# Kernel tuning notes

Measured on AMD Instinct MI355X. Metric: run time of the kernel, lower is better.

The kernel has to match this reference:

```python
import jax, jax.numpy as jnp
import numpy as np

B, L, LQ = 64, 4096, 128
D = 32        # input_dim (value channels)
ET = 128      # embed_time
NH = 1        # num_heads
H = 128       # nhidden
NC = 6        # n_classes


def _time_emb(tt, lin_w, lin_b, per_w, per_b):
    # tt [..., T] -> [..., T, ET]; cat(Linear(1,1)(t), sin(Linear(1,ET-1)(t)))
    tt = tt[..., None]
    out1 = tt * lin_w[0, 0] + lin_b
    out2 = jnp.sin(tt @ per_w + per_b)
    return jnp.concatenate([out1, out2], axis=-1)


def _gru_dir(xs, wih, whh, bih, bhh, reverse):
    # xs [B, T, I] -> [B, T, H]; torch GRU gate math
    xs_t = jnp.swapaxes(xs, 0, 1)              # [T, B, I]
    if reverse:
        xs_t = xs_t[::-1]
    gi_all = xs_t @ wih.T + bih                # [T, B, 3H] precomputed input gates
    h0 = jnp.zeros((xs.shape[0], H), xs.dtype)

    def step(h, gi):
        gh = h @ whh.T + bhh
        ir, iz, inn = jnp.split(gi, 3, axis=-1)
        hr, hz, hn = jnp.split(gh, 3, axis=-1)
        r = jax.nn.sigmoid(ir + hr)
        z = jax.nn.sigmoid(iz + hz)
        n = jnp.tanh(inn + r * hn)
        h_new = (1.0 - z) * n + z * h
        return h_new, h_new

    _, ys = jax.lax.scan(step, h0, gi_all)     # [T, B, H]
    if reverse:
        ys = ys[::-1]
    return jnp.swapaxes(ys, 0, 1)


def _bigru(xs, wih, whh, bih, bhh):
    fwd = _gru_dir(xs, wih[0], whh[0], bih[0], bhh[0], False)
    bwd = _gru_dir(xs, wih[1], whh[1], bih[1], bhh[1], True)
    return jnp.concatenate([fwd, bwd], axis=-1)


def setup_inputs() -> dict:
    ks = jax.random.split(jax.random.key(0), 32)
    w = lambda i, s: jax.random.normal(ks[i], s, jnp.float32) * 0.05
    G3 = 3 * H
    return {
        "x": jax.random.normal(ks[0], (B, L, D), jnp.float32),
        "time_steps": jax.random.uniform(ks[1], (B, L), dtype=jnp.float32),
        "query_times": jnp.linspace(0.0, 1.0, LQ, dtype=jnp.float32),
        "lin_w": w(2, (1, 1)), "lin_b": w(3, (1,)),
        "per_w": w(4, (1, ET - 1)), "per_b": w(5, (ET - 1,)),
        "wq": w(6, (ET, ET)), "bq": w(7, (ET,)),
        "wk": w(8, (ET, ET)), "bk": w(9, (ET,)),
        "wo": w(10, (NH * D, H)), "bo": w(11, (H,)),
        "gru0_wih": w(12, (2, G3, H)), "gru0_whh": w(13, (2, G3, H)),
        "gru0_bih": w(14, (2, G3)), "gru0_bhh": w(15, (2, G3)),
        "gru1_wih": w(16, (2, G3, 2 * H)), "gru1_whh": w(17, (2, G3, H)),
        "gru1_bih": w(18, (2, G3)), "gru1_bhh": w(19, (2, G3)),
        "c1_w": w(20, (2 * H, 128)), "c1_b": w(21, (128,)),
        "c2_w": w(22, (128, 64)), "c2_b": w(23, (64,)),
        "c3_w": w(24, (64, NC)), "c3_b": w(25, (NC,)),
    }


def reference(x, time_steps, query_times, lin_w, lin_b, per_w, per_b,
              wq, bq, wk, bk, wo, bo,
              gru0_wih, gru0_whh, gru0_bih, gru0_bhh,
              gru1_wih, gru1_whh, gru1_bih, gru1_bhh,
              c1_w, c1_b, c2_w, c2_b, c3_w, c3_b):
    ek = ET // NH
    # learned time embeddings
    q = _time_emb(query_times[None, :], lin_w, lin_b, per_w, per_b)  # [1, LQ, ET]
    k = _time_emb(time_steps, lin_w, lin_b, per_w, per_b)            # [B, L, ET]
    # per-head projections
    qp = (q @ wq + bq).reshape(1, LQ, NH, ek).transpose(0, 2, 1, 3)[0]  # [NH, LQ, ek]
    kp = (k @ wk + bk).reshape(B, L, NH, ek).transpose(0, 2, 1, 3)      # [B, NH, L, ek]
    # mTAN attention: scores are channel-independent (mask=None), so the
    # per-channel repeat+softmax reduces to a single softmax over keys.
    scores = jnp.einsum('hqe,bhke->bhqk', qp, kp) / jnp.sqrt(jnp.float32(ek))
    p = jax.nn.softmax(scores, axis=-1)                                 # [B, NH, LQ, L]
    att = jnp.einsum('bhqk,bkd->bqhd', p, x).reshape(B, LQ, NH * D)
    att_out = att @ wo + bo                                             # [B, LQ, H]
    # 2-layer bidirectional GRU
    g0 = _bigru(att_out, gru0_wih, gru0_whh, gru0_bih, gru0_bhh)        # [B, LQ, 2H]
    g1 = _bigru(g0, gru1_wih, gru1_whh, gru1_bih, gru1_bhh)             # [B, LQ, 2H]
    class_in = jnp.concatenate([g1[:, -1, :H], g1[:, 0, H:]], axis=1)   # [B, 2H]
    out = ((class_in @ c1_w + c1_b) @ c2_w + c2_b) @ c3_w + c3_b        # [B, NC]
    return out
```

## Files before the change

kernel.cpp:

```cpp
#include <hip/hip_runtime.h>
#include <math.h>

#define Bn   64
#define Ln   4096
#define LQn  128
#define Dn   32
#define ETn  128
#define Hn   128
#define G3n  384
#define NDEG 12

typedef __attribute__((ext_vector_type(2))) float f32x2;
typedef __attribute__((ext_vector_type(2))) _Float16 f16x2;

#define DPPF(x, ctrl) __int_as_float(__builtin_amdgcn_update_dpp(0, __float_as_int(x), (ctrl), 0xF, 0xF, true))
#define QP_XOR1 0xB1
#define QP_XOR2 0x4E
#define QP_B0   0x00
#define QP_B1   0x55
#define QP_B2   0xAA
#define QP_B3   0xFF

__device__ __forceinline__ float sin_poly(float x) {
    const float x2 = x * x;
    float r = -1.9841270114e-04f;
    r = fmaf(r, x2,  8.3333337680e-03f);
    r = fmaf(r, x2, -1.6666667163e-01f);
    return fmaf(r * x2, x, x);
}
__device__ __forceinline__ float cos_poly(float x) {
    const float x2 = x * x;
    float r =  2.4801587642e-05f;
    r = fmaf(r, x2, -1.3888888899e-03f);
    r = fmaf(r, x2,  4.1666667908e-02f);
    r = fmaf(r, x2, -5.0000000000e-01f);
    return fmaf(r, x2, 1.0f);
}

#define WS_C    0
#define WS_WT   4096
#define WS_B2   (WS_WT + 768*32)
#define WS_CLS  (WS_B2 + 1024)
#define WS_G0   (WS_CLS + Bn*2*Hn)
#define WS_GI   (WS_G0 + Bn*LQn*2*Hn)
#define WS_ACCP WS_G0
#define WS_SP   (WS_G0 + 1048576)

__global__ __launch_bounds__(128) void k_coef(
    const float* __restrict__ qtimes, const float* __restrict__ lin_w,
    const float* __restrict__ lin_b, const float* __restrict__ per_w,
    const float* __restrict__ per_b, const float* __restrict__ wq,
    const float* __restrict__ bq, const float* __restrict__ wk,
    const float* __restrict__ bk, float* __restrict__ C)
{
    __shared__ float qe[ETn], qp_l[ETn], qt_l[ETn], bas[NDEG * 128], red[96], qbk_red[32];
    const int q = blockIdx.x, tid = threadIdx.x;
    if (tid < ETn - 1) {
        const float w = per_w[tid], bb = per_b[tid];
        const float sb = sin_poly(bb), cb = cos_poly(bb);
        float wp = 1.f;
#pragma unroll
        for (int d = 0; d < NDEG; ++d) {
            const float sd = ((d & 3) == 0) ? sb : ((d & 3) == 1) ? cb : ((d & 3) == 2) ? -sb : -cb;
            bas[d * 128 + tid] = wp * sd;
            wp *= w / (float)(d + 1);
        }
    }
    const float t = qtimes[q];
    qe[tid] = (tid == 0) ? fmaf(t, lin_w[0], lin_b[0])
                         : sin_poly(fmaf(t, per_w[tid - 1], per_b[tid - 1]));
    __syncthreads();
    {
        float a = bq[tid];
#pragma unroll 16
        for (int i = 0; i < ETn; ++i) a = fmaf(qe[i], wq[i * ETn + tid], a);
        qp_l[tid] = a;
    }
    __syncthreads();
    {
        const float4* wk4 = (const float4*)(wk + (size_t)tid * ETn);
        const float4* qp4 = (const float4*)qp_l;
        float a = 0.f;
#pragma unroll
        for (int k = 0; k < 32; ++k) {
            const float4 w4 = wk4[k], p4 = qp4[k];
            a += w4.x * p4.x + w4.y * p4.y + w4.z * p4.z + w4.w * p4.w;
        }
        qt_l[tid] = a;
    }
    __syncthreads();
    if (tid < 96) {
        const int d = tid >> 3, g = tid & 7;
        float p = 0.f;
        for (int j = g; j < ETn - 1; j += 8) p = fmaf(qt_l[j + 1], bas[d * 128 + j], p);
        red[tid] = p;
    } else {
        const int g2 = tid - 96;
        float p = 0.f;
#pragma unroll
        for (int k = 0; k < 4; ++k) p = fmaf(qp_l[g2 + 32 * k], bk[g2 + 32 * k], p);
        qbk_red[g2] = p;
    }
    __syncthreads();
    if (tid < NDEG) {
        const int d = tid;
        float s = red[d * 8 + 0] + red[d * 8 + 1] + red[d * 8 + 2] + red[d * 8 + 3]
                + red[d * 8 + 4] + red[d * 8 + 5] + red[d * 8 + 6] + red[d * 8 + 7];
        if (d == 0) {
            float qbk = 0.f;
#pragma unroll
            for (int k = 0; k < 32; ++k) qbk += qbk_red[k];
            s += qt_l[0] * lin_b[0] + qbk;
        }
        if (d == 1) s += qt_l[0] * lin_w[0];
        C[q * NDEG + d] = s * 0.08838834764831845f;
    }
}

__global__ __launch_bounds__(256) void k_fuse(
    const float* __restrict__ wih, const float* __restrict__ wo,
    const float* __restrict__ bo, const float* __restrict__ bih,
    float* __restrict__ Wt, float* __restrict__ bias2)
{
    const int t = blockIdx.x * 256 + threadIdx.x;
    if (t < 768 * 32) {
        const int o = t >> 5, d = t & 31;
        const float4* wr4 = (const float4*)(wih + (size_t)o * 128);
        const float4* wc4 = (const float4*)(wo + (size_t)d * 128);
        float a = 0.f;
#pragma unroll
        for (int k = 0; k < 32; ++k) {
            const float4 r4 = wr4[k], c4 = wc4[k];
            a += r4.x * c4.x + r4.y * c4.y + r4.z * c4.z + r4.w * c4.w;
        }
        Wt[t] = a;
    } else if (t < 768 * 33) {
        const int o = t - 768 * 32;
        const float4* wr4 = (const float4*)(wih + (size_t)o * 128);
        const float4* bo4 = (const float4*)bo;
        float a = bih[o];
#pragma unroll
        for (int k = 0; k < 32; ++k) {
            const float4 r4 = wr4[k], b4 = bo4[k];
            a += r4.x * b4.x + r4.y * b4.y + r4.z * b4.z + r4.w * b4.w;
        }
        bias2[o] = a;
    }
}

__global__ __launch_bounds__(512, 1) void k_attn(
    const float* __restrict__ x, const float* __restrict__ tsteps,
    const float* __restrict__ Cc, float* __restrict__ accP, float* __restrict__ sP)
{
    __shared__ float4 xls[4 * 64 * 8];
    __shared__ float  slab[4][128][36];
    const int tid = threadIdx.x;
    const int b = blockIdx.x >> 2, lsplit = blockIdx.x & 3;
    const int i = tid & 3, qt = (tid >> 2) & 31, ls2 = tid >> 7;
    const int qown = 4 * qt + i;
    const int u = tid & 127;

    float c[NDEG];
#pragma unroll
    for (int d = 0; d < NDEG; ++d) c[d] = Cc[qown * NDEG + d];

    const int l0 = lsplit * 1024 + ls2 * 256;
    const float4* tg4 = (const float4*)(tsteps + (size_t)b * Ln + l0);
    const float4* xg  = (const float4*)(x + ((size_t)b * Ln + l0) * Dn);

    f32x2 acc2[4][4];
#pragma unroll
    for (int m = 0; m < 4; ++m)
#pragma unroll
        for (int e = 0; e < 4; ++e) { acc2[m][e].x = 0.f; acc2[m][e].y = 0.f; }
    float s_own = 0.f;

    float4 xr[4];
#pragma unroll
    for (int w = 0; w < 4; ++w) xr[w] = xg[u + 128 * w];

    for (int ch = 0; ch < 4; ++ch) {
        __syncthreads();
#pragma unroll
        for (int w = 0; w < 4; ++w) xls[ls2 * 512 + u + 128 * w] = xr[w];
        __syncthreads();
        if (ch < 3) {
            const int off = (ch + 1) * 512;
#pragma unroll
            for (int w = 0; w < 4; ++w) xr[w] = xg[off + u + 128 * w];
        }
        const float4* xrow = &xls[ls2 * 512];
        for (int k = 0; k < 16; ++k) {
            const float4 t4 = tg4[ch * 16 + k];
#pragma unroll
            for (int jj = 0; jj < 4; ++jj) {
                const float t = (jj == 0) ? t4.x : (jj == 1) ? t4.y : (jj == 2) ? t4.z : t4.w;
                float sc = c[NDEG - 1];
#pragma unroll
                for (int d = NDEG - 2; d >= 0; --d) sc = fmaf(sc, t, c[d]);
                const float pe = __expf(sc);
                s_own += pe;
                const float p0 = DPPF(pe, QP_B0);
                const float p1 = DPPF(pe, QP_B1);
                const float p2 = DPPF(pe, QP_B2);
                const float p3 = DPPF(pe, QP_B3);
                const int lrow = (k * 4 + jj) * 8;
                const float4 xa = xrow[lrow + 2 * i];
                const float4 xb = xrow[lrow + 2 * i + 1];
                f32x2 xa0; xa0.x = xa.x; xa0.y = xa.y;
                f32x2 xa1; xa1.x = xa.z; xa1.y = xa.w;
                f32x2 xb0; xb0.x = xb.x; xb0.y = xb.y;
                f32x2 xb1; xb1.x = xb.z; xb1.y = xb.w;
#define PKA(m, pv) { f32x2 pp; pp.x = (pv); pp.y = (pv); \
    acc2[m][0] = __builtin_elementwise_fma(pp, xa0, acc2[m][0]); \
    acc2[m][1] = __builtin_elementwise_fma(pp, xa1, acc2[m][1]); \
    acc2[m][2] = __builtin_elementwise_fma(pp, xb0, acc2[m][2]); \
    acc2[m][3] = __builtin_elementwise_fma(pp, xb1, acc2[m][3]); }
                PKA(0, p0) PKA(1, p1) PKA(2, p2) PKA(3, p3)
#undef PKA
            }
        }
    }
    __syncthreads();
#pragma unroll
    for (int m = 0; m < 4; ++m) {
        float4 f4a, f4b;
        f4a.x = acc2[m][0].x; f4a.y = acc2[m][0].y; f4a.z = acc2[m][1].x; f4a.w = acc2[m][1].y;
        f4b.x = acc2[m][2].x; f4b.y = acc2[m][2].y; f4b.z = acc2[m][3].x; f4b.w = acc2[m][3].y;
        *(float4*)&slab[ls2][4 * qt + m][8 * i]     = f4a;
        *(float4*)&slab[ls2][4 * qt + m][8 * i + 4] = f4b;
    }
    slab[ls2][qown][32] = s_own;
    __syncthreads();
    const int q = tid & 127, part = tid >> 7;
#pragma unroll
    for (int j = 0; j < 2; ++j) {
        const int off = (part * 2 + j) * 4;
        float4 r  = *(float4*)&slab[0][q][off];
        float4 r1 = *(float4*)&slab[1][q][off];
        float4 r2 = *(float4*)&slab[2][q][off];
        float4 r3 = *(float4*)&slab[3][q][off];
        r.x += r1.x + r2.x + r3.x; r.y += r1.y + r2.y + r3.y;
        r.z += r1.z + r2.z + r3.z; r.w += r1.w + r2.w + r3.w;
        *(float4*)&accP[((((size_t)lsplit * Bn + b) * LQn + q) * 32) + off] = r;
    }
    if (part == 0) {
        sP[((size_t)lsplit * Bn + b) * LQn + q] =
            slab[0][q][32] + slab[1][q][32] + slab[2][q][32] + slab[3][q][32];
    }
}

__global__ __launch_bounds__(256) void k_gemm_att(
    const float* __restrict__ accP, const float* __restrict__ sP,
    const float* __restrict__ Bm, const float* __restrict__ bias,
    float* __restrict__ Cm)
{
    __shared__ float4 A_l[64 * 8];
    __shared__ float4 B_l[64 * 8];
    const int tid = threadIdx.x;
    const int m0 = blockIdx.x * 64, n0 = blockIdx.y * 64;
    const int r0 = (tid >> 4) << 2, c0 = (tid & 15) << 2;
    f32x2 acc2[4][4];
#pragma unroll
    for (int a = 0; a < 4; ++a)
#pragma unroll
        for (int bb = 0; bb < 4; ++bb) { acc2[a][bb].x = 0.f; acc2[a][bb].y = 0.f; }
    const float4* Ag = (const float4*)accP;
    const float4* Bg = (const float4*)Bm;

#pragma unroll
    for (int w = 0; w < 2; ++w) {
        const int idx = tid + w * 256;
        const int row = idx >> 3, c4 = idx & 7;
        const int sc = (c4 + row + (row >> 2)) & 7;
        const int m = m0 + row;
        float4 a0 = Ag[(size_t)m * 8 + c4];
        float4 a1 = Ag[((size_t)8192  + m) * 8 + c4];
        float4 a2 = Ag[((size_t)16384 + m) * 8 + c4];
        float4 a3 = Ag[((size_t)24576 + m) * 8 + c4];
        const float inv = 1.f / (sP[m] + sP[8192 + m] + sP[16384 + m] + sP[24576 + m]);
        float4 av;
        av.x = (a0.x + a1.x + a2.x + a3.x) * inv;
        av.y = (a0.y + a1.y + a2.y + a3.y) * inv;
        av.z = (a0.z + a1.z + a2.z + a3.z) * inv;
        av.w = (a0.w + a1.w + a2.w + a3.w) * inv;
        A_l[row * 8 + sc] = av;
        B_l[row * 8 + sc] = Bg[(size_t)(n0 + row) * 8 + c4];
    }
    __syncthreads();
#pragma unroll
    for (int k4 = 0; k4 < 8; ++k4) {
        float4 av[4], bv[4];
#pragma unroll
        for (int j = 0; j < 4; ++j) {
            const int ra = r0 + j;
            av[j] = A_l[ra * 8 + ((k4 + ra + (ra >> 2)) & 7)];
        }
#pragma unroll
        for (int j = 0; j < 4; ++j) {
            const int rb = c0 + j;
            bv[j] = B_l[rb * 8 + ((k4 + rb + (rb >> 2)) & 7)];
        }
#pragma unroll
        for (int ri = 0; ri < 4; ++ri) {
            f32x2 alo; alo.x = av[ri].x; alo.y = av[ri].y;
            f32x2 ahi; ahi.x = av[ri].z; ahi.y = av[ri].w;
#pragma unroll
            for (int ci = 0; ci < 4; ++ci) {
                f32x2 blo; blo.x = bv[ci].x; blo.y = bv[ci].y;
                f32x2 bhi; bhi.x = bv[ci].z; bhi.y = bv[ci].w;
                acc2[ri][ci] = __builtin_elementwise_fma(alo, blo, acc2[ri][ci]);
                acc2[ri][ci] = __builtin_elementwise_fma(ahi, bhi, acc2[ri][ci]);
            }
        }
    }
#pragma unroll
    for (int ri = 0; ri < 4; ++ri) {
        float4 o4;
        o4.x = acc2[ri][0].x + acc2[ri][0].y + bias[n0 + c0 + 0];
        o4.y = acc2[ri][1].x + acc2[ri][1].y + bias[n0 + c0 + 1];
        o4.z = acc2[ri][2].x + acc2[ri][2].y + bias[n0 + c0 + 2];
        o4.w = acc2[ri][3].x + acc2[ri][3].y + bias[n0 + c0 + 3];
        *(float4*)&Cm[(size_t)(m0 + r0 + ri) * 768 + n0 + c0] = o4;
    }
}

__global__ __launch_bounds__(256) void k_gemm_nt(
    const float* __restrict__ A, const float* __restrict__ Bm,
    const float* __restrict__ bias, float* __restrict__ Cm,
    int N, int K)
{
    __shared__ float4 A_l[64 * 8];
    __shared__ float4 B_l[64 * 8];
    const int tid = threadIdx.x;
    const int m0 = blockIdx.x * 64, n0 = blockIdx.y * 64;
    const int r0 = (tid >> 4) << 2, c0 = (tid & 15) << 2;
    const int K4 = K >> 2;
    f32x2 acc2[4][4];
#pragma unroll
    for (int a = 0; a < 4; ++a)
#pragma unroll
        for (int bb = 0; bb < 4; ++bb) { acc2[a][bb].x = 0.f; acc2[a][bb].y = 0.f; }
    const float4* Ag = (const float4*)A;
    const float4* Bg = (const float4*)Bm;

    for (int k0 = 0; k0 < K4; k0 += 8) {
        __syncthreads();
#pragma unroll
        for (int w = 0; w < 2; ++w) {
            const int idx = tid + w * 256;
            const int row = idx >> 3, c4 = idx & 7;
            const int sc = (c4 + row + (row >> 2)) & 7;
            A_l[row * 8 + sc] = Ag[(size_t)(m0 + row) * K4 + k0 + c4];
            B_l[row * 8 + sc] = Bg[(size_t)(n0 + row) * K4 + k0 + c4];
        }
        __syncthreads();
#pragma unroll
        for (int k4 = 0; k4 < 8; ++k4) {
            float4 av[4], bv[4];
#pragma unroll
            for (int j = 0; j < 4; ++j) {
                const int ra = r0 + j;
                av[j] = A_l[ra * 8 + ((k4 + ra + (ra >> 2)) & 7)];
            }
#pragma unroll
            for (int j = 0; j < 4; ++j) {
                const int rb = c0 + j;
                bv[j] = B_l[rb * 8 + ((k4 + rb + (rb >> 2)) & 7)];
            }
#pragma unroll
            for (int ri = 0; ri < 4; ++ri) {
                f32x2 alo; alo.x = av[ri].x; alo.y = av[ri].y;
                f32x2 ahi; ahi.x = av[ri].z; ahi.y = av[ri].w;
#pragma unroll
                for (int ci = 0; ci < 4; ++ci) {
                    f32x2 blo; blo.x = bv[ci].x; blo.y = bv[ci].y;
                    f32x2 bhi; bhi.x = bv[ci].z; bhi.y = bv[ci].w;
                    acc2[ri][ci] = __builtin_elementwise_fma(alo, blo, acc2[ri][ci]);
                    acc2[ri][ci] = __builtin_elementwise_fma(ahi, bhi, acc2[ri][ci]);
                }
            }
        }
    }
#pragma unroll
    for (int ri = 0; ri < 4; ++ri) {
        float4 o4;
        o4.x = acc2[ri][0].x + acc2[ri][0].y + bias[n0 + c0 + 0];
        o4.y = acc2[ri][1].x + acc2[ri][1].y + bias[n0 + c0 + 1];
        o4.z = acc2[ri][2].x + acc2[ri][2].y + bias[n0 + c0 + 2];
        o4.w = acc2[ri][3].x + acc2[ri][3].y + bias[n0 + c0 + 3];
        *(float4*)&Cm[(size_t)(m0 + r0 + ri) * N + n0 + c0] = o4;
    }
}

__global__ __launch_bounds__(512) void k_gru(
    const float* __restrict__ gi, const float* __restrict__ whh,
    const float* __restrict__ bhh, float* __restrict__ seq_out,
    float* __restrict__ final_out)
{
    __shared__ _Float16 h16[2][Hn];
    __shared__ float    h32[2][Hn];
    const int tid = threadIdx.x;
    const int b = blockIdx.x >> 1, dir = blockIdx.x & 1;
    const int j = tid >> 2, q = tid & 3;

    f16x2 wr[16], wz[16], wn[16];
    {
        const float* wb = whh + ((size_t)dir * G3n + j) * Hn + 32 * q;
        const f32x2* p0 = (const f32x2*)(wb);
        const f32x2* p1 = (const f32x2*)(wb + (size_t)128 * Hn);
        const f32x2* p2 = (const f32x2*)(wb + (size_t)256 * Hn);
#pragma unroll
        for (int k = 0; k < 16; ++k) {
            f32x2 a = p0[k], bz2 = p1[k], c2 = p2[k];
            wr[k].x = (_Float16)a.x;   wr[k].y = (_Float16)a.y;
            wz[k].x = (_Float16)bz2.x; wz[k].y = (_Float16)bz2.y;
            wn[k].x = (_Float16)c2.x;  wn[k].y = (_Float16)c2.y;
        }
    }
#pragma unroll
    for (int k = 0; k < 16; ++k) {
        asm volatile("" : "+v"(wr[k]));
        asm volatile("" : "+v"(wz[k]));
        asm volatile("" : "+v"(wn[k]));
    }
    const float bhr = bhh[dir * G3n + j];
    const float bhz = bhh[dir * G3n + 128 + j];
    const float bhn = bhh[dir * G3n + 256 + j];

    if (tid < 2 * Hn) { ((_Float16*)h16)[tid] = (_Float16)0.f; ((float*)h32)[tid] = 0.f; }
    __syncthreads();

    const long sstride = dir ? -768 : 768;
    const float* gptr = gi + (size_t)b * LQn * 768 + dir * G3n + q * Hn + j
                        + (size_t)(dir ? LQn - 1 : 0) * 768;
    const bool ldq = (q < 3);

    int cur = 0;
    float hlast = 0.f;

    auto gstep = [&](const float gi_cur, const int step) {
        const float hold = h32[cur][j];
        const float4* hb4 = (const float4*)(&h16[cur][32 * q]);
        float sr = 0.f, sz = 0.f, sn = 0.f;
#pragma unroll
        for (int k2 = 0; k2 < 4; ++k2) {
            float4 hv = hb4[k2];
            f16x2 h0 = *(f16x2*)&hv.x;
            f16x2 h1 = *(f16x2*)&hv.y;
            f16x2 h2 = *(f16x2*)&hv.z;
            f16x2 h3 = *(f16x2*)&hv.w;
            asm("v_dot2_f32_f16 %0, %1, %2, %0" : "+v"(sr) : "v"(wr[4 * k2 + 0]), "v"(h0));
            asm("v_dot2_f32_f16 %0, %1, %2, %0" : "+v"(sz) : "v"(wz[4 * k2 + 0]), "v"(h0));
            asm("v_dot2_f32_f16 %0, %1, %2, %0" : "+v"(sn) : "v"(wn[4 * k2 + 0]), "v"(h0));
            asm("v_dot2_f32_f16 %0, %1, %2, %0" : "+v"(sr) : "v"(wr[4 * k2 + 1]), "v"(h1));
            asm("v_dot2_f32_f16 %0, %1, %2, %0" : "+v"(sz) : "v"(wz[4 * k2 + 1]), "v"(h1));
            asm("v_dot2_f32_f16 %0, %1, %2, %0" : "+v"(sn) : "v"(wn[4 * k2 + 1]), "v"(h1));
            asm("v_dot2_f32_f16 %0, %1, %2, %0" : "+v"(sr) : "v"(wr[4 * k2 + 2]), "v"(h2));
            asm("v_dot2_f32_f16 %0, %1, %2, %0" : "+v"(sz) : "v"(wz[4 * k2 + 2]), "v"(h2));
            asm("v_dot2_f32_f16 %0, %1, %2, %0" : "+v"(sn) : "v"(wn[4 * k2 + 2]), "v"(h2));
            asm("v_dot2_f32_f16 %0, %1, %2, %0" : "+v"(sr) : "v"(wr[4 * k2 + 3]), "v"(h3));
            asm("v_dot2_f32_f16 %0, %1, %2, %0" : "+v"(sz) : "v"(wz[4 * k2 + 3]), "v"(h3));
            asm("v_dot2_f32_f16 %0, %1, %2, %0" : "+v"(sn) : "v"(wn[4 * k2 + 3]), "v"(h3));
        }
        sr += DPPF(sr, QP_XOR1); sr += DPPF(sr, QP_XOR2);
        sz += DPPF(sz, QP_XOR1); sz += DPPF(sz, QP_XOR2);
        sn += DPPF(sn, QP_XOR1); sn += DPPF(sn, QP_XOR2);
        const float gir = DPPF(gi_cur, QP_B0);
        const float giz = DPPF(gi_cur, QP_B1);
        const float gin = DPPF(gi_cur, QP_B2);
        const float r = 1.f / (1.f + __expf(-(gir + sr + bhr)));
        const float z = 1.f / (1.f + __expf(-(giz + sz + bhz)));
        const float nx = gin + r * (sn + bhn);
        const float n = 1.f - 2.f / (1.f + __expf(2.f * nx));
        const float hn = n + z * (hold - n);
        if (q == 0) {
            h32[cur ^ 1][j] = hn;
            h16[cur ^ 1][j] = (_Float16)hn;
        }
        if (q == 3) {
            if (seq_out) {
                const int l = dir ? (LQn - 1 - step) : step;
                seq_out[((size_t)(b * LQn + l)) * (2 * Hn) + dir * Hn + j] = hn;
            }
            hlast = hn;
        }
        cur ^= 1;
        asm volatile("s_waitcnt lgkmcnt(0)\n\ts_barrier" ::: "memory");
    };

    float gA, gB, gC, gD;
#define GLD(d, s) { d = ldq ? gptr[(long)(s) * sstride] : 0.f; }
    GLD(gA, 0) GLD(gB, 1) GLD(gC, 2) GLD(gD, 3)
    for (int s0 = 0; s0 < LQn; s0 += 4) {
        gstep(gA, s0);
        { const int sn2 = (s0 + 4 < LQn) ? s0 + 4 : LQn - 1; GLD(gA, sn2) }
        gstep(gB, s0 + 1);
        { const int sn2 = (s0 + 5 < LQn) ? s0 + 5 : LQn - 1; GLD(gB, sn2) }
        gstep(gC, s0 + 2);
        { const int sn2 = (s0 + 6 < LQn) ? s0 + 6 : LQn - 1; GLD(gC, sn2) }
        gstep(gD, s0 + 3);
        { const int sn2 = (s0 + 7 < LQn) ? s0 + 7 : LQn - 1; GLD(gD, sn2) }
    }
#undef GLD
    if (final_out && q == 3) final_out[b * 2 * Hn + dir * Hn + j] = hlast;
}

__global__ __launch_bounds__(256) void k_cls(
    const float* __restrict__ cls_in,
    const float* __restrict__ c1w, const float* __restrict__ c1b,
    const float* __restrict__ c2w, const float* __restrict__ c2b,
    const float* __restrict__ c3w, const float* __restrict__ c3b,
    float* __restrict__ out)
{
    __shared__ float ci[256], y1[128], y2[64];
    const int b = blockIdx.x, tid = threadIdx.x;
    ci[tid] = cls_in[b * 256 + tid];
    __syncthreads();
    if (tid < 128) { float a = c1b[tid]; for (int i = 0; i < 256; ++i) a += ci[i] * c1w[i * 128 + tid]; y1[tid] = a; }
    __syncthreads();
    if (tid < 64)  { float a = c2b[tid]; for (int i = 0; i < 128; ++i) a += y1[i] * c2w[i * 64 + tid];  y2[tid] = a; }
    __syncthreads();
    if (tid < 6)   { float a = c3b[tid]; for (int i = 0; i < 64; ++i)  a += y2[i] * c3w[i * 6 + tid];   out[b * 6 + tid] = a; }
}

extern "C" void kernel_launch(void* const* d_in, const int* in_sizes, int n_in,
                              void* d_out, int out_size, void* d_ws, size_t ws_size,
                              hipStream_t stream)
{
    const float* x        = (const float*)d_in[0];
    const float* tsteps   = (const float*)d_in[1];
    const float* qtimes   = (const float*)d_in[2];
    const float* lin_w    = (const float*)d_in[3];
    const float* lin_b    = (const float*)d_in[4];
    const float* per_w    = (const float*)d_in[5];
    const float* per_b    = (const float*)d_in[6];
    const float* wq       = (const float*)d_in[7];
    const float* bq       = (const float*)d_in[8];
    const float* wk       = (const float*)d_in[9];
    const float* bk       = (const float*)d_in[10];
    const float* wo       = (const float*)d_in[11];
    const float* bo       = (const float*)d_in[12];
    const float* g0_wih   = (const float*)d_in[13];
    const float* g0_whh   = (const float*)d_in[14];
    const float* g0_bih   = (const float*)d_in[15];
    const float* g0_bhh   = (const float*)d_in[16];
    const float* g1_wih   = (const float*)d_in[17];
    const float* g1_whh   = (const float*)d_in[18];
    const float* g1_bih   = (const float*)d_in[19];
    const float* g1_bhh   = (const float*)d_in[20];
    const float* c1w      = (const float*)d_in[21];
    const float* c1b      = (const float*)d_in[22];
    const float* c2w      = (const float*)d_in[23];
    const float* c2b      = (const float*)d_in[24];
    const float* c3w      = (const float*)d_in[25];
    const float* c3b      = (const float*)d_in[26];
    float* out = (float*)d_out;
    float* ws  = (float*)d_ws;

    float* Cws   = ws + WS_C;
    float* Wt    = ws + WS_WT;
    float* bias2 = ws + WS_B2;
    float* clsin = ws + WS_CLS;
    float* g0buf = ws + WS_G0;
    float* accP  = ws + WS_ACCP;
    float* sPb   = ws + WS_SP;
    float* gibuf = ws + WS_GI;

    k_coef<<<128, 128, 0, stream>>>(qtimes, lin_w, lin_b, per_w, per_b, wq, bq, wk, bk, Cws);
    k_fuse<<<99, 256, 0, stream>>>(g0_wih, wo, bo, g0_bih, Wt, bias2);
    k_attn<<<256, 512, 0, stream>>>(x, tsteps, Cws, accP, sPb);

    k_gemm_att<<<dim3(128, 12), 256, 0, stream>>>(accP, sPb, Wt, bias2, gibuf);
    k_gru<<<128, 512, 0, stream>>>(gibuf, g0_whh, g0_bhh, g0buf, nullptr);

    k_gemm_nt<<<dim3(128, 12), 256, 0, stream>>>(g0buf, g1_wih, g1_bih, gibuf, 768, 256);
    k_gru<<<128, 512, 0, stream>>>(gibuf, g1_whh, g1_bhh, nullptr, clsin);

    k_cls<<<64, 256, 0, stream>>>(clsin, c1w, c1b, c2w, c2b, c3w, c3b, out);
}
```

Measured before the change: 332.1 us.

## Split GRU hidden dot products over two lanes per unit instead of four

The recurrent GRU kernel now uses 256 threads per block, with two lanes per hidden unit each covering 64 inputs, instead of 512 threads with four lanes each covering 32. Each lane holds twice as many fp16 weight registers, the reduction drops to one DPP step, and every lane loads its own three input-gate values, so the DPP broadcasts are gone. The aim is to shorten the per-step cross-lane and barrier work on the serial critical path. The cost is a longer serial dot-product chain per lane and higher register pressure.

```diff
diff --git a/kernel.cpp b/kernel.cpp
--- a/kernel.cpp
+++ b/kernel.cpp
@@ -393,7 +393,7 @@
     }
 }
 
-__global__ __launch_bounds__(512) void k_gru(
+__global__ __launch_bounds__(256, 1) void k_gru(
     const float* __restrict__ gi, const float* __restrict__ whh,
     const float* __restrict__ bhh, float* __restrict__ seq_out,
     float* __restrict__ final_out)
@@ -402,24 +402,24 @@
     __shared__ float    h32[2][Hn];
     const int tid = threadIdx.x;
     const int b = blockIdx.x >> 1, dir = blockIdx.x & 1;
-    const int j = tid >> 2, q = tid & 3;
-
-    f16x2 wr[16], wz[16], wn[16];
+    const int j = tid >> 1, q = tid & 1;
+
+    f16x2 wr[32], wz[32], wn[32];
     {
-        const float* wb = whh + ((size_t)dir * G3n + j) * Hn + 32 * q;
+        const float* wb = whh + ((size_t)dir * G3n + j) * Hn + 64 * q;
         const f32x2* p0 = (const f32x2*)(wb);
         const f32x2* p1 = (const f32x2*)(wb + (size_t)128 * Hn);
         const f32x2* p2 = (const f32x2*)(wb + (size_t)256 * Hn);
 #pragma unroll
-        for (int k = 0; k < 16; ++k) {
-            f32x2 a = p0[k], bz2 = p1[k], c2 = p2[k];
-            wr[k].x = (_Float16)a.x;   wr[k].y = (_Float16)a.y;
-            wz[k].x = (_Float16)bz2.x; wz[k].y = (_Float16)bz2.y;
-            wn[k].x = (_Float16)c2.x;  wn[k].y = (_Float16)c2.y;
-        }
-    }
-#pragma unroll
-    for (int k = 0; k < 16; ++k) {
+        for (int k = 0; k < 32; ++k) {
+            f32x2 a = p0[k], z2 = p1[k], c2 = p2[k];
+            wr[k].x = (_Float16)a.x;  wr[k].y = (_Float16)a.y;
+            wz[k].x = (_Float16)z2.x; wz[k].y = (_Float16)z2.y;
+            wn[k].x = (_Float16)c2.x; wn[k].y = (_Float16)c2.y;
+        }
+    }
+#pragma unroll
+    for (int k = 0; k < 32; ++k) {
         asm volatile("" : "+v"(wr[k]));
         asm volatile("" : "+v"(wz[k]));
         asm volatile("" : "+v"(wn[k]));
@@ -428,23 +428,25 @@
     const float bhz = bhh[dir * G3n + 128 + j];
     const float bhn = bhh[dir * G3n + 256 + j];
 
-    if (tid < 2 * Hn) { ((_Float16*)h16)[tid] = (_Float16)0.f; ((float*)h32)[tid] = 0.f; }
+    if (tid < Hn) {
+        h32[0][tid] = 0.f; h32[1][tid] = 0.f;
+        h16[0][tid] = (_Float16)0.f; h16[1][tid] = (_Float16)0.f;
+    }
     __syncthreads();
 
     const long sstride = dir ? -768 : 768;
-    const float* gptr = gi + (size_t)b * LQn * 768 + dir * G3n + q * Hn + j
+    const float* gptr = gi + (size_t)b * LQn * 768 + dir * G3n + j
                         + (size_t)(dir ? LQn - 1 : 0) * 768;
-    const bool ldq = (q < 3);
 
     int cur = 0;
     float hlast = 0.f;
 
-    auto gstep = [&](const float gi_cur, const int step) {
+    auto gstep = [&](const float gir, const float giz, const float gin, const int step) {
         const float hold = h32[cur][j];
-        const float4* hb4 = (const float4*)(&h16[cur][32 * q]);
+        const float4* hb4 = (const float4*)(&h16[cur][64 * q]);
         float sr = 0.f, sz = 0.f, sn = 0.f;
 #pragma unroll
-        for (int k2 = 0; k2 < 4; ++k2) {
+        for (int k2 = 0; k2 < 8; ++k2) {
             float4 hv = hb4[k2];
             f16x2 h0 = *(f16x2*)&hv.x;
             f16x2 h1 = *(f16x2*)&hv.y;
@@ -463,12 +465,9 @@
             asm("v_dot2_f32_f16 %0, %1, %2, %0" : "+v"(sz) : "v"(wz[4 * k2 + 3]), "v"(h3));
             asm("v_dot2_f32_f16 %0, %1, %2, %0" : "+v"(sn) : "v"(wn[4 * k2 + 3]), "v"(h3));
         }
-        sr += DPPF(sr, QP_XOR1); sr += DPPF(sr, QP_XOR2);
-        sz += DPPF(sz, QP_XOR1); sz += DPPF(sz, QP_XOR2);
-        sn += DPPF(sn, QP_XOR1); sn += DPPF(sn, QP_XOR2);
-        const float gir = DPPF(gi_cur, QP_B0);
-        const float giz = DPPF(gi_cur, QP_B1);
-        const float gin = DPPF(gi_cur, QP_B2);
+        sr += DPPF(sr, QP_XOR1);
+        sz += DPPF(sz, QP_XOR1);
+        sn += DPPF(sn, QP_XOR1);
         const float r = 1.f / (1.f + __expf(-(gir + sr + bhr)));
         const float z = 1.f / (1.f + __expf(-(giz + sz + bhz)));
         const float nx = gin + r * (sn + bhn);
@@ -477,33 +476,28 @@
         if (q == 0) {
             h32[cur ^ 1][j] = hn;
             h16[cur ^ 1][j] = (_Float16)hn;
-        }
-        if (q == 3) {
             if (seq_out) {
                 const int l = dir ? (LQn - 1 - step) : step;
                 seq_out[((size_t)(b * LQn + l)) * (2 * Hn) + dir * Hn + j] = hn;
             }
-            hlast = hn;
-        }
+        }
+        hlast = hn;
         cur ^= 1;
         asm volatile("s_waitcnt lgkmcnt(0)\n\ts_barrier" ::: "memory");
     };
 
-    float gA, gB, gC, gD;
-#define GLD(d, s) { d = ldq ? gptr[(long)(s) * sstride] : 0.f; }
-    GLD(gA, 0) GLD(gB, 1) GLD(gC, 2) GLD(gD, 3)
-    for (int s0 = 0; s0 < LQn; s0 += 4) {
-        gstep(gA, s0);
-        { const int sn2 = (s0 + 4 < LQn) ? s0 + 4 : LQn - 1; GLD(gA, sn2) }
-        gstep(gB, s0 + 1);
-        { const int sn2 = (s0 + 5 < LQn) ? s0 + 5 : LQn - 1; GLD(gB, sn2) }
-        gstep(gC, s0 + 2);
-        { const int sn2 = (s0 + 6 < LQn) ? s0 + 6 : LQn - 1; GLD(gC, sn2) }
-        gstep(gD, s0 + 3);
-        { const int sn2 = (s0 + 7 < LQn) ? s0 + 7 : LQn - 1; GLD(gD, sn2) }
+    float gA[3], gB[3];
+#define GLD(dst, s) { const long o = (long)(s) * sstride; \
+    dst[0] = gptr[o]; dst[1] = gptr[o + 128]; dst[2] = gptr[o + 256]; }
+    GLD(gA, 0) GLD(gB, 1)
+    for (int s0 = 0; s0 < LQn; s0 += 2) {
+        gstep(gA[0], gA[1], gA[2], s0);
+        { const int sn2 = (s0 + 2 < LQn) ? s0 + 2 : LQn - 1; GLD(gA, sn2) }
+        gstep(gB[0], gB[1], gB[2], s0 + 1);
+        { const int sn2 = (s0 + 3 < LQn) ? s0 + 3 : LQn - 1; GLD(gB, sn2) }
     }
 #undef GLD
-    if (final_out && q == 3) final_out[b * 2 * Hn + dir * Hn + j] = hlast;
+    if (final_out && q == 0) final_out[b * 2 * Hn + dir * Hn + j] = hlast;
 }
 
 __global__ __launch_bounds__(256) void k_cls(
@@ -572,10 +566,10 @@
     k_attn<<<256, 512, 0, stream>>>(x, tsteps, Cws, accP, sPb);
 
     k_gemm_att<<<dim3(128, 12), 256, 0, stream>>>(accP, sPb, Wt, bias2, gibuf);
-    k_gru<<<128, 512, 0, stream>>>(gibuf, g0_whh, g0_bhh, g0buf, nullptr);
+    k_gru<<<128, 256, 0, stream>>>(gibuf, g0_whh, g0_bhh, g0buf, nullptr);
 
     k_gemm_nt<<<dim3(128, 12), 256, 0, stream>>>(g0buf, g1_wih, g1_bih, gibuf, 768, 256);
-    k_gru<<<128, 512, 0, stream>>>(gibuf, g1_whh, g1_bhh, nullptr, clsin);
+    k_gru<<<128, 256, 0, stream>>>(gibuf, g1_whh, g1_bhh, nullptr, clsin);
 
     k_cls<<<64, 256, 0, stream>>>(clsin, c1w, c1b, c2w, c2b, c3w, c3b, out);
 }
```

Measured after the change: 302.3 us. 9.0% less time.
